# Kernel optimization log

Measured on AMD Instinct MI355X. Metric: run time of the kernel, lower is better.

The kernel has to match this reference:

```python
import jax, jax.numpy as jnp
import numpy as np
from jax import lax

R = 2            # search_range
S = 2 * R + 1    # window extent per axis
NCH = S ** 3     # output channels (125)


def _offset_table():
    # Loop order matches the original triple loop (i over H, j over W, h over D).
    # Channel index (S*i + S*j + h) may be negative -> Python negative indexing,
    starts, chans = [], []
    for i in range(-R, R + 1):          # H shift
        for j in range(-R, R + 1):      # W shift
            for h in range(-R, R + 1):  # D shift
                # out[a] = sum_c x1[a] * x2[a - shift]; padded start = R - shift
                starts.append((R - h, R - i, R - j))
                chans.append((S * i + S * j + h) % NCH)
    src = np.full(NCH, -1, dtype=np.int64)
    for t, c in enumerate(chans):
        src[c] = t
    return np.asarray(starts, np.int32), src


def setup_inputs() -> dict:
    key = jax.random.key(0)
    k1, k2 = jax.random.split(key)
    B, C, D, H, W = 2, 64, 32, 64, 64
    x1 = jax.random.normal(k1, (B, C, D, H, W), dtype=jnp.float32)
    x2 = jax.random.normal(k2, (B, C, D, H, W), dtype=jnp.float32)
    return {"x1": x1, "x2": x2}


def reference(x1, x2):
    B, C, D, H, W = x1.shape
    starts_np, src_np = _offset_table()
    starts = jnp.asarray(starts_np)                          # [NCH, 3]
    # zero-pad x2 so every shifted window is a static-size slice
    x2p = jnp.pad(x2, ((0, 0), (0, 0), (R, R), (R, R), (R, R)))

    def corr(off):
        x2s = lax.dynamic_slice(x2p, (0, 0, off[0], off[1], off[2]),
                                (B, C, D, H, W))
        return jnp.einsum('bcdhw,bcdhw->bdhw', x1, x2s)

    corrs = lax.map(corr, starts)                            # [NCH, B, D, H, W]
    src = jnp.asarray(src_np)
    written = (src >= 0)[:, None, None, None, None]
    cv = jnp.where(written, corrs[jnp.clip(src, 0)], jnp.float32(0.0))
    return jnp.transpose(cv, (1, 0, 2, 3, 4)) / NCH          # [B, NCH, D, H, W]
```

## Files before the change

kernel.cpp:

```cpp
#include <hip/hip_runtime.h>

#define B_ 2
#define C_ 64
#define D_ 32
#define H_ 64
#define W_ 64
#define NCH 125
#define HW_ 4096
#define DHW_ 131072
#define CDHW_ 8388608

#define BSTR 68
#define TROWS 8
#define TBUF (TROWS * BSTR)
#define WLDS (2 * TBUF)

__device__ __attribute__((aligned(16))) const float g_zero[4] = {0.f, 0.f, 0.f, 0.f};

__global__ __launch_bounds__(128, 5) void cv_all(const float* __restrict__ x1,
                                                 const float* __restrict__ x2,
                                                 float* __restrict__ out)
{
    __shared__ __align__(16) float lds[2 * WLDS];

    const int tx   = threadIdx.x;
    const int ty   = threadIdx.y;
    const int tid  = ty * 16 + tx;
    const int lane = tid & 63;
    const int w    = tid >> 6;

    const int lin     = blockIdx.x;
    const int logical = (lin & 7) * 320 + (lin >> 3);
    const int bz   = logical % 10;
    const int rest = logical / 10;
    const int y0   = (rest & 7) * 8;
    const int d    = rest >> 3;
    const int b    = bz / 5;
    const int hi   = bz - b * 5;
    const int hh   = hi - 2;
    const int y    = y0 + ty;
    const int x    = tx * 4;
    const int zd   = d - hh;
    const bool zok = (zd >= 0) && (zd < D_);

    const float* x2b = x2 + (size_t)b * CDHW_ + (size_t)(zok ? zd : 0) * HW_;
    const int lrA = lane >> 4,        qA = lane & 15;
    const int lrB = (lane + 64) >> 4, qB = lane & 15;
    const int grA = y0 + 4 * w - 2 + lrA;
    const int grB = y0 + 4 * w - 2 + lrB;
    const bool vA = zok && (grA >= 0) && (grA < H_);
    const bool vB = zok && (grB < H_);
    const float* pA = vA ? (x2b + grA * W_ + 4 * qA) : g_zero;
    const float* pB = vB ? (x2b + grB * W_ + 4 * qB) : g_zero;

    const int wbase = w * WLDS;
    const int dA = lrA * BSTR + 2 + 4 * qA;
    const int dB = lrB * BSTR + 2 + 4 * qB;

    {
        const int half = lane >> 5, rem = lane & 31;
        const int hr = rem >> 2, hc = rem & 3;
        const int hidx = (hc < 2) ? hc : (64 + hc);
        lds[wbase + half * TBUF + hr * BSTR + hidx] = 0.f;
    }

    const float* p1 = x1 + (size_t)b * CDHW_ + (size_t)d * HW_ + (y * W_ + x);
    const int lr0 = ty & 3;

    float4 a0 = *(const float4*)p1;
    float4 a1 = *(const float4*)(p1 + DHW_);
    float4 a2 = *(const float4*)(p1 + 2 * DHW_);
    const float4 L0a = *(const float4*)pA;
    const float4 L0b = *(const float4*)pB;
    float4 SWa = *(const float4*)(pA + (vA ? DHW_ : 0));
    float4 SWb = *(const float4*)(pB + (vB ? DHW_ : 0));
    float4 SFa = *(const float4*)(pA + (vA ? 2 * DHW_ : 0));
    float4 SFb = *(const float4*)(pB + (vB ? 2 * DHW_ : 0));
    {
        float* Wb = lds + wbase;
        *(float2*)(Wb + dA)     = make_float2(L0a.x, L0a.y);
        *(float2*)(Wb + dA + 2) = make_float2(L0a.z, L0a.w);
        *(float2*)(Wb + dB)     = make_float2(L0b.x, L0b.y);
        *(float2*)(Wb + dB + 2) = make_float2(L0b.z, L0b.w);
    }

    float acc[9][4];
#pragma unroll
    for (int k = 0; k < 9; ++k)
#pragma unroll
        for (int j = 0; j < 4; ++j) acc[k][j] = 0.f;

#pragma unroll 2
    for (int c = 0; c < C_; ++c) {
        float* Wb = lds + wbase + ((c + 1) & 1) * TBUF;
        *(float2*)(Wb + dA)     = make_float2(SWa.x, SWa.y);
        *(float2*)(Wb + dA + 2) = make_float2(SWa.z, SWa.w);
        *(float2*)(Wb + dB)     = make_float2(SWb.x, SWb.y);
        *(float2*)(Wb + dB + 2) = make_float2(SWb.z, SWb.w);
        SWa = SFa; SWb = SFb;

        const int off = ((c + 3) & 63) * DHW_;
        SFa = *(const float4*)(pA + (vA ? off : 0));
        SFb = *(const float4*)(pB + (vB ? off : 0));
        const float4 a = a0;
        a0 = a1; a1 = a2;
        a2 = *(const float4*)(p1 + off);

        const float* Bb = lds + wbase + (c & 1) * TBUF;
        float4 k0;
#pragma unroll
        for (int k = 0; k < 5; ++k) {
            const float4 c4 = *(const float4*)(Bb + (lr0 + k) * BSTR + x + 4);
            if (k == 0) k0 = c4;
            const int ai = 4 - k;
            acc[ai][0] += a.x * c4.x;
            acc[ai][1] += a.y * c4.y;
            acc[ai][2] += a.z * c4.z;
            acc[ai][3] += a.w * c4.w;
        }
        const float4 rl = *(const float4*)(Bb + lr0 * BSTR + x);
        const float r8[8] = {rl.x, rl.y, rl.z, rl.w, k0.x, k0.y, k0.z, k0.w};
#pragma unroll
        for (int s = 1; s <= 4; ++s) {
            const int ai = s + 4;
            acc[ai][0] += a.x * r8[4 - s];
            acc[ai][1] += a.y * r8[5 - s];
            acc[ai][2] += a.z * r8[6 - s];
            acc[ai][3] += a.w * r8[7 - s];
        }
    }

    float* ob = out + (size_t)b * NCH * DHW_ + (size_t)d * HW_ + (y * W_ + x);
    const float inv = 1.0f / 125.0f;
#pragma unroll
    for (int k = 0; k < 9; ++k) {
        const int s = k - 4;
        int ch = 5 * s + hh;
        ch = (ch % NCH + NCH) % NCH;
        float4 v;
        v.x = acc[k][0] * inv;
        v.y = acc[k][1] * inv;
        v.z = acc[k][2] * inv;
        v.w = acc[k][3] * inv;
        *(float4*)(ob + (size_t)ch * DHW_) = v;
    }
    const float4 zero4 = make_float4(0.f, 0.f, 0.f, 0.f);
#pragma unroll
    for (int t = 0; t < 16; ++t) {
        const int ch = 23 + hi * 16 + t;
        *(float4*)(ob + (size_t)ch * DHW_) = zero4;
    }
}

extern "C" void kernel_launch(void* const* d_in, const int* in_sizes, int n_in,
                              void* d_out, int out_size, void* d_ws, size_t ws_size,
                              hipStream_t stream) {
    const float* x1 = (const float*)d_in[0];
    const float* x2 = (const float*)d_in[1];
    float* out = (float*)d_out;
    cv_all<<<dim3(2560, 1, 1), dim3(16, 8, 1), 0, stream>>>(x1, x2, out);
}
```

Before: 275.6 us.

## Load x2 halo tiles directly into LDS with triple-buffered async copies

Replaces the register-staged x2 prefetch and ds_write path with global_load_lds direct-to-LDS copies into a three-stage ring buffer, synchronised with an explicit vmcnt wait. The padded LDS row stride goes away and the horizontal halo is handled by masking edge lanes to zero. The zero-channel stores are spread across the channel loop instead of being issued at the end. This aims to cut VGPR pressure and LDS write instructions and to overlap output writes with compute, but it relies on a hand-tuned waitcnt and on wave-local ordering without barriers, which is fragile.

```diff
diff --git a/kernel.cpp b/kernel.cpp
--- a/kernel.cpp
+++ b/kernel.cpp
@@ -10,24 +10,29 @@
 #define DHW_ 131072
 #define CDHW_ 8388608
 
-#define BSTR 68
 #define TROWS 8
-#define TBUF (TROWS * BSTR)
-#define WLDS (2 * TBUF)
+#define TBUF (TROWS * W_)
+#define WREG (3 * TBUF)
 
 __device__ __attribute__((aligned(16))) const float g_zero[4] = {0.f, 0.f, 0.f, 0.f};
+
+__device__ __forceinline__ void glds16(const float* g, float* l) {
+    __builtin_amdgcn_global_load_lds(
+        (const __attribute__((address_space(1))) void*)g,
+        (__attribute__((address_space(3))) void*)l, 16, 0, 0);
+}
 
 __global__ __launch_bounds__(128, 5) void cv_all(const float* __restrict__ x1,
                                                  const float* __restrict__ x2,
                                                  float* __restrict__ out)
 {
-    __shared__ __align__(16) float lds[2 * WLDS];
+    __shared__ __align__(16) float lds[4 + 2 * WREG + 4];
 
-    const int tx   = threadIdx.x;
-    const int ty   = threadIdx.y;
-    const int tid  = ty * 16 + tx;
+    const int tid  = threadIdx.y * 16 + threadIdx.x;
     const int lane = tid & 63;
     const int w    = tid >> 6;
+    const int tx   = lane & 15;
+    const int lr0  = lane >> 4;
 
     const int lin     = blockIdx.x;
     const int logical = (lin & 7) * 320 + (lin >> 3);
@@ -38,51 +43,34 @@
     const int b    = bz / 5;
     const int hi   = bz - b * 5;
     const int hh   = hi - 2;
-    const int y    = y0 + ty;
+    const int y0w  = y0 + 4 * w;
+    const int y    = y0w + lr0;
     const int x    = tx * 4;
     const int zd   = d - hh;
     const bool zok = (zd >= 0) && (zd < D_);
 
     const float* x2b = x2 + (size_t)b * CDHW_ + (size_t)(zok ? zd : 0) * HW_;
-    const int lrA = lane >> 4,        qA = lane & 15;
-    const int lrB = (lane + 64) >> 4, qB = lane & 15;
-    const int grA = y0 + 4 * w - 2 + lrA;
-    const int grB = y0 + 4 * w - 2 + lrB;
-    const bool vA = zok && (grA >= 0) && (grA < H_);
+    const int q   = lane & 15;
+    const int grA = y0w - 2 + (lane >> 4);
+    const int grB = y0w + 2 + (lane >> 4);
+    const bool vA = zok && (grA >= 0);
     const bool vB = zok && (grB < H_);
-    const float* pA = vA ? (x2b + grA * W_ + 4 * qA) : g_zero;
-    const float* pB = vB ? (x2b + grB * W_ + 4 * qB) : g_zero;
+    const float* pA = vA ? (x2b + grA * W_ + 4 * q) : g_zero;
+    const float* pB = vB ? (x2b + grB * W_ + 4 * q) : g_zero;
+    const int sA = vA ? DHW_ : 0;
+    const int sB = vB ? DHW_ : 0;
 
-    const int wbase = w * WLDS;
-    const int dA = lrA * BSTR + 2 + 4 * qA;
-    const int dB = lrB * BSTR + 2 + 4 * qB;
+    const int wbase = 4 + w * WREG;
+    const float* p1 = x1 + (size_t)b * CDHW_ + (size_t)d * HW_ + (y * W_ + x);
 
-    {
-        const int half = lane >> 5, rem = lane & 31;
-        const int hr = rem >> 2, hc = rem & 3;
-        const int hidx = (hc < 2) ? hc : (64 + hc);
-        lds[wbase + half * TBUF + hr * BSTR + hidx] = 0.f;
-    }
+    float* obz = out + (size_t)b * NCH * DHW_ + (size_t)(23 + hi * 16) * DHW_
+                     + (size_t)d * HW_ + (y * W_ + x);
+    const float4 zero4 = make_float4(0.f, 0.f, 0.f, 0.f);
 
-    const float* p1 = x1 + (size_t)b * CDHW_ + (size_t)d * HW_ + (y * W_ + x);
-    const int lr0 = ty & 3;
-
+    glds16(pA, lds + wbase);
+    glds16(pB, lds + wbase + TBUF / 2);
     float4 a0 = *(const float4*)p1;
-    float4 a1 = *(const float4*)(p1 + DHW_);
-    float4 a2 = *(const float4*)(p1 + 2 * DHW_);
-    const float4 L0a = *(const float4*)pA;
-    const float4 L0b = *(const float4*)pB;
-    float4 SWa = *(const float4*)(pA + (vA ? DHW_ : 0));
-    float4 SWb = *(const float4*)(pB + (vB ? DHW_ : 0));
-    float4 SFa = *(const float4*)(pA + (vA ? 2 * DHW_ : 0));
-    float4 SFb = *(const float4*)(pB + (vB ? 2 * DHW_ : 0));
-    {
-        float* Wb = lds + wbase;
-        *(float2*)(Wb + dA)     = make_float2(L0a.x, L0a.y);
-        *(float2*)(Wb + dA + 2) = make_float2(L0a.z, L0a.w);
-        *(float2*)(Wb + dB)     = make_float2(L0b.x, L0b.y);
-        *(float2*)(Wb + dB + 2) = make_float2(L0b.z, L0b.w);
-    }
+    pA += sA; pB += sB;
 
     float acc[9][4];
 #pragma unroll
@@ -90,44 +78,57 @@
 #pragma unroll
         for (int j = 0; j < 4; ++j) acc[k][j] = 0.f;
 
+    const bool lo_edge = (tx == 0);
+    const bool hi_edge = (tx == 15);
+
 #pragma unroll 2
     for (int c = 0; c < C_; ++c) {
-        float* Wb = lds + wbase + ((c + 1) & 1) * TBUF;
-        *(float2*)(Wb + dA)     = make_float2(SWa.x, SWa.y);
-        *(float2*)(Wb + dA + 2) = make_float2(SWa.z, SWa.w);
-        *(float2*)(Wb + dB)     = make_float2(SWb.x, SWb.y);
-        *(float2*)(Wb + dB + 2) = make_float2(SWb.z, SWb.w);
-        SWa = SFa; SWb = SFb;
+        float* dst = lds + wbase + ((c + 1) % 3) * TBUF;
+        glds16(pA, dst);
+        glds16(pB, dst + TBUF / 2);
+        float4 a1 = *(const float4*)(p1 + (size_t)((c + 1) & 63) * DHW_);
+        if (c < 62) { pA += sA; pB += sB; }
 
-        const int off = ((c + 3) & 63) * DHW_;
-        SFa = *(const float4*)(pA + (vA ? off : 0));
-        SFb = *(const float4*)(pB + (vB ? off : 0));
+        asm volatile("s_waitcnt vmcnt(3)" ::: "memory");
+
+        const float* Bb = lds + wbase + (c % 3) * TBUF;
         const float4 a = a0;
-        a0 = a1; a1 = a2;
-        a2 = *(const float4*)(p1 + off);
-
-        const float* Bb = lds + wbase + (c & 1) * TBUF;
-        float4 k0;
+        float2 k0A, k0B;
 #pragma unroll
         for (int k = 0; k < 5; ++k) {
-            const float4 c4 = *(const float4*)(Bb + (lr0 + k) * BSTR + x + 4);
-            if (k == 0) k0 = c4;
+            const float* pr = Bb + (lr0 + k) * W_ + x;
+            const float2 cA = *(const float2*)(pr + 2);
+            float2 cB = *(const float2*)(pr + 4);
+            cB.x = hi_edge ? 0.f : cB.x;
+            cB.y = hi_edge ? 0.f : cB.y;
+            if (k == 0) { k0A = cA; k0B = cB; }
             const int ai = 4 - k;
-            acc[ai][0] += a.x * c4.x;
-            acc[ai][1] += a.y * c4.y;
-            acc[ai][2] += a.z * c4.z;
-            acc[ai][3] += a.w * c4.w;
+            acc[ai][0] += a.x * cA.x;
+            acc[ai][1] += a.y * cA.y;
+            acc[ai][2] += a.z * cB.x;
+            acc[ai][3] += a.w * cB.y;
         }
-        const float4 rl = *(const float4*)(Bb + lr0 * BSTR + x);
-        const float r8[8] = {rl.x, rl.y, rl.z, rl.w, k0.x, k0.y, k0.z, k0.w};
+        {
+            const float* pr = Bb + lr0 * W_ + x;
+            float2 rlA = *(const float2*)(pr - 2);
+            const float2 rlB = *(const float2*)(pr);
+            rlA.x = lo_edge ? 0.f : rlA.x;
+            rlA.y = lo_edge ? 0.f : rlA.y;
+            const float r8[8] = {rlA.x, rlA.y, rlB.x, rlB.y,
+                                 k0A.x, k0A.y, k0B.x, k0B.y};
 #pragma unroll
-        for (int s = 1; s <= 4; ++s) {
-            const int ai = s + 4;
-            acc[ai][0] += a.x * r8[4 - s];
-            acc[ai][1] += a.y * r8[5 - s];
-            acc[ai][2] += a.z * r8[6 - s];
-            acc[ai][3] += a.w * r8[7 - s];
+            for (int s = 1; s <= 4; ++s) {
+                const int ai = s + 4;
+                acc[ai][0] += a.x * r8[4 - s];
+                acc[ai][1] += a.y * r8[5 - s];
+                acc[ai][2] += a.z * r8[6 - s];
+                acc[ai][3] += a.w * r8[7 - s];
+            }
         }
+        a0 = a1;
+
+        if ((c & 3) == 0)
+            *(float4*)(obz + (size_t)(c >> 2) * DHW_) = zero4;
     }
 
     float* ob = out + (size_t)b * NCH * DHW_ + (size_t)d * HW_ + (y * W_ + x);
@@ -144,12 +145,6 @@
         v.w = acc[k][3] * inv;
         *(float4*)(ob + (size_t)ch * DHW_) = v;
     }
-    const float4 zero4 = make_float4(0.f, 0.f, 0.f, 0.f);
-#pragma unroll
-    for (int t = 0; t < 16; ++t) {
-        const int ch = 23 + hi * 16 + t;
-        *(float4*)(ob + (size_t)ch * DHW_) = zero4;
-    }
 }
 
 extern "C" void kernel_launch(void* const* d_in, const int* in_sizes, int n_in,
```

Measured after the change: 268.9 us. 2.5% less time.
